# Performance work log

Measured on AMD Instinct MI355X. Metric: run time of the kernel, lower is better.

## Reference

```python
import jax, jax.numpy as jnp
import numpy as np

CROP = 14          # initial_crop_size
POOL_K = 2         # maxpool_kernel_size == maxpool_stride


def setup_inputs() -> dict:
    key = jax.random.key(0)
    k1, k2 = jax.random.split(key)
    features = jax.random.normal(k1, (1, 50, 50, 1024), dtype=jnp.float32)
    raw = jax.random.uniform(k2, (1, 300, 4), dtype=jnp.float32)
    # well-formed normalized boxes: y1<=y2, x1<=x2
    ys = jnp.sort(raw[..., 0::2], axis=-1)
    xs = jnp.sort(raw[..., 1::2], axis=-1)
    boxes = jnp.stack([ys[..., 0], xs[..., 0], ys[..., 1], xs[..., 1]], axis=-1)
    return {"features": features, "boxes": boxes}


def _crop_and_resize(feat, boxes, crop_size):
    # feat: [H, W, C]; boxes: [N, 4] normalized (y1, x1, y2, x2)
    # Matches tf.image.crop_and_resize bilinear semantics for crop_size > 1.
    H, W, _ = feat.shape
    y1, x1, y2, x2 = boxes[:, 0], boxes[:, 1], boxes[:, 2], boxes[:, 3]
    grid = jnp.arange(crop_size, dtype=feat.dtype)  # [S]
    # sample coordinates in source pixel space: [N, S]
    ys = y1[:, None] * (H - 1) + grid[None, :] * ((y2 - y1) * (H - 1) / (crop_size - 1))[:, None]
    xs = x1[:, None] * (W - 1) + grid[None, :] * ((x2 - x1) * (W - 1) / (crop_size - 1))[:, None]
    y0f = jnp.floor(ys)
    x0f = jnp.floor(xs)
    wy = (ys - y0f)[:, :, None, None]  # [N, S, 1, 1]
    wx = (xs - x0f)[:, None, :, None]  # [N, 1, S, 1]
    y0 = jnp.clip(y0f.astype(jnp.int32), 0, H - 1)
    y1i = jnp.clip(y0 + 1, 0, H - 1)
    x0 = jnp.clip(x0f.astype(jnp.int32), 0, W - 1)
    x1i = jnp.clip(x0 + 1, 0, W - 1)
    # four corner gathers -> [N, S, S, C]
    tl = feat[y0[:, :, None], x0[:, None, :]]
    tr = feat[y0[:, :, None], x1i[:, None, :]]
    bl = feat[y1i[:, :, None], x0[:, None, :]]
    br = feat[y1i[:, :, None], x1i[:, None, :]]
    top = tl + (tr - tl) * wx
    bot = bl + (br - bl) * wx
    return top + (bot - top) * wy


def reference(features, boxes):
    # features: [1, H, W, C]; boxes: [1, N, 4]
    crops = _crop_and_resize(features[0], boxes[0], CROP)  # [N, 14, 14, C]
    N, S, _, C = crops.shape
    P = S // POOL_K
    # 2x2 stride-2 max pool (kernel == stride, S even)
    pooled = crops.reshape(N, P, POOL_K, P, POOL_K, C).max(axis=(2, 4))  # [N, 7, 7, C]
    return pooled[None]  # [1, N, 7, 7, C]
```

## Files before the change

kernel.cpp:

```cpp
#include <hip/hip_runtime.h>
#include <math.h>

#define FH 50
#define FW 50
#define FC 1024
#define FC4 256
#define NBOX 300
#define PO 7
#define CHQ 4
#define NPIX (FH * FW * FC)
#define BF16_BYTES (NPIX * 2)

typedef float nat4 __attribute__((ext_vector_type(4)));

__device__ __forceinline__ nat4 lerp4(nat4 a, nat4 b, float w) {
    return a + (b - a) * w;
}
__device__ __forceinline__ nat4 max4(nat4 a, nat4 b) {
    nat4 r;
    r.x = fmaxf(a.x, b.x);
    r.y = fmaxf(a.y, b.y);
    r.z = fmaxf(a.z, b.z);
    r.w = fmaxf(a.w, b.w);
    return r;
}
__device__ __forceinline__ nat4 bf2f(uint2 u) {
    nat4 r;
    r.x = __uint_as_float(u.x << 16);
    r.y = __uint_as_float(u.x & 0xffff0000u);
    r.z = __uint_as_float(u.y << 16);
    r.w = __uint_as_float(u.y & 0xffff0000u);
    return r;
}
__device__ __forceinline__ unsigned bfpack(float a, float b) {
    unsigned ua = __float_as_uint(a);
    unsigned ub = __float_as_uint(b);
    ua += 0x7fffu + ((ua >> 16) & 1u);
    ub += 0x7fffu + ((ub >> 16) & 1u);
    return (ua >> 16) | (ub & 0xffff0000u);
}

__global__ __launch_bounds__(256) void cvt_kernel(
    const float* __restrict__ feat, unsigned* __restrict__ ws)
{
    const int i = blockIdx.x * 256 + threadIdx.x;
    const float4 v = reinterpret_cast<const float4*>(feat)[i];
    uint2 w;
    w.x = bfpack(v.x, v.y);
    w.y = bfpack(v.z, v.w);
    reinterpret_cast<uint2*>(ws)[i] = w;
}

__global__ __launch_bounds__(64) void roi_pool_bf16_kernel(
    const unsigned* __restrict__ ws,
    const float* __restrict__ boxes,
    float* __restrict__ out)
{
    const int j = blockIdx.x & 7;
    const int k = blockIdx.x >> 3;
    const int n = j + 8 * (k / (PO * CHQ));
    if (n >= NBOX) return;
    const int r  = k % (PO * CHQ);
    const int py = r >> 2;
    const int cq = r & 3;
    const int c  = cq * 64 + threadIdx.x;

    const float by1 = boxes[n * 4 + 0];
    const float bx1 = boxes[n * 4 + 1];
    const float by2 = boxes[n * 4 + 2];
    const float bx2 = boxes[n * 4 + 3];

    const float stepy = (by2 - by1) * (49.0f / 13.0f);
    const float stepx = (bx2 - bx1) * (49.0f / 13.0f);
    const float basey = by1 * 49.0f;
    const float basex = bx1 * 49.0f;

    const float ysA = basey + (float)(2 * py) * stepy;
    const float ysB = ysA + stepy;
    const float fA = floorf(ysA); const float wyA = ysA - fA;
    const float fB = floorf(ysB); const float wyB = ysB - fB;
    const int y0A = min(max((int)fA, 0), FH - 1); const int y1A = min(y0A + 1, FH - 1);
    const int y0B = min(max((int)fB, 0), FH - 1); const int y1B = min(y0B + 1, FH - 1);

    const uint2* __restrict__ f2 = reinterpret_cast<const uint2*>(ws);
    const int r0 = y0A * FW, r1 = y1A * FW, r2 = y0B * FW, r3 = y1B * FW;

    uint2 c00, c01, c10, c11, c20, c21, c30, c31;
    uint2 n00, n01, n10, n11, n20, n21, n30, n31;

    int cc;
    {
        const float xf = floorf(basex);
        cc = min(max((int)xf, 0), FW - 1);
        const int x1 = min(cc + 1, FW - 1);
        c00 = f2[(r0 + cc) * FC4 + c];  c01 = f2[(r0 + x1) * FC4 + c];
        c10 = f2[(r1 + cc) * FC4 + c];  c11 = f2[(r1 + x1) * FC4 + c];
        c20 = f2[(r2 + cc) * FC4 + c];  c21 = f2[(r2 + x1) * FC4 + c];
        c30 = f2[(r3 + cc) * FC4 + c];  c31 = f2[(r3 + x1) * FC4 + c];
    }

    nat4 m = (nat4)(-INFINITY);
    nat4* __restrict__ obase =
        reinterpret_cast<nat4*>(out) + (size_t)(n * (PO * PO) + py * PO) * FC4 + c;

    for (int ix = 0; ix < 2 * PO; ++ix) {
        int d = 0;
        if (ix < 2 * PO - 1) {
            const float xsn = basex + (float)(ix + 1) * stepx;
            const int nx0 = min(max((int)floorf(xsn), 0), FW - 1);
            const int nx1 = min(nx0 + 1, FW - 1);
            d = nx0 - cc;
            if (d == 1) {
                n01 = f2[(r0 + nx1) * FC4 + c];
                n11 = f2[(r1 + nx1) * FC4 + c];
                n21 = f2[(r2 + nx1) * FC4 + c];
                n31 = f2[(r3 + nx1) * FC4 + c];
            } else if (d >= 2) {
                n00 = f2[(r0 + nx0) * FC4 + c];  n01 = f2[(r0 + nx1) * FC4 + c];
                n10 = f2[(r1 + nx0) * FC4 + c];  n11 = f2[(r1 + nx1) * FC4 + c];
                n20 = f2[(r2 + nx0) * FC4 + c];  n21 = f2[(r2 + nx1) * FC4 + c];
                n30 = f2[(r3 + nx0) * FC4 + c];  n31 = f2[(r3 + nx1) * FC4 + c];
            }
            cc = nx0;
        }

        {
            const float xs = basex + (float)ix * stepx;
            const float wx = xs - floorf(xs);
            const nat4 vA = lerp4(lerp4(bf2f(c00), bf2f(c01), wx),
                                  lerp4(bf2f(c10), bf2f(c11), wx), wyA);
            const nat4 vB = lerp4(lerp4(bf2f(c20), bf2f(c21), wx),
                                  lerp4(bf2f(c30), bf2f(c31), wx), wyB);
            m = max4(m, max4(vA, vB));
        }

        if (ix & 1) {
            __builtin_nontemporal_store(m, obase + (ix >> 1) * FC4);
            m = (nat4)(-INFINITY);
        }

        if (ix < 2 * PO - 1) {
            if (d == 1) {
                c00 = c01; c10 = c11; c20 = c21; c30 = c31;
                c01 = n01; c11 = n11; c21 = n21; c31 = n31;
            } else if (d >= 2) {
                c00 = n00; c01 = n01; c10 = n10; c11 = n11;
                c20 = n20; c21 = n21; c30 = n30; c31 = n31;
            }
        }
    }
}

__global__ __launch_bounds__(64) void roi_pool_f32_kernel(
    const float* __restrict__ feat,
    const float* __restrict__ boxes,
    float* __restrict__ out)
{
    const int j = blockIdx.x & 7;
    const int k = blockIdx.x >> 3;
    const int n = j + 8 * (k / (PO * CHQ));
    if (n >= NBOX) return;
    const int r  = k % (PO * CHQ);
    const int py = r >> 2;
    const int cq = r & 3;
    const int c4 = cq * 64 + threadIdx.x;

    const float by1 = boxes[n * 4 + 0];
    const float bx1 = boxes[n * 4 + 1];
    const float by2 = boxes[n * 4 + 2];
    const float bx2 = boxes[n * 4 + 3];
    const float stepy = (by2 - by1) * (49.0f / 13.0f);
    const float stepx = (bx2 - bx1) * (49.0f / 13.0f);
    const float basey = by1 * 49.0f;
    const float basex = bx1 * 49.0f;
    const float ysA = basey + (float)(2 * py) * stepy;
    const float ysB = ysA + stepy;
    const float fA = floorf(ysA); const float wyA = ysA - fA;
    const float fB = floorf(ysB); const float wyB = ysB - fB;
    const int y0A = min(max((int)fA, 0), FH - 1); const int y1A = min(y0A + 1, FH - 1);
    const int y0B = min(max((int)fB, 0), FH - 1); const int y1B = min(y0B + 1, FH - 1);

    const nat4* __restrict__ f4 = reinterpret_cast<const nat4*>(feat);
    const int rA0 = y0A * FW, rA1 = y1A * FW, rB0 = y0B * FW, rB1 = y1B * FW;

    int cc = -1000;
    nat4 A00, A01, A10, A11, B00, B01, B10, B11;
    A00 = A01 = A10 = A11 = B00 = B01 = B10 = B11 = (nat4)0.0f;
    nat4 m = (nat4)(-INFINITY);
    nat4* __restrict__ obase =
        reinterpret_cast<nat4*>(out) + (size_t)(n * (PO * PO) + py * PO) * FC4 + c4;

    for (int ix = 0; ix < 2 * PO; ++ix) {
        const float xs = basex + (float)ix * stepx;
        const float xf = floorf(xs);
        const float wx = xs - xf;
        int x0 = min(max((int)xf, 0), FW - 1);
        const int x1 = min(x0 + 1, FW - 1);
        if (x0 != cc) {
            if (x0 == cc + 1) {
                A00 = A01; A10 = A11; B00 = B01; B10 = B11;
                A01 = f4[(rA0 + x1) * FC4 + c4];
                A11 = f4[(rA1 + x1) * FC4 + c4];
                B01 = f4[(rB0 + x1) * FC4 + c4];
                B11 = f4[(rB1 + x1) * FC4 + c4];
            } else {
                A00 = f4[(rA0 + x0) * FC4 + c4];
                A01 = f4[(rA0 + x1) * FC4 + c4];
                A10 = f4[(rA1 + x0) * FC4 + c4];
                A11 = f4[(rA1 + x1) * FC4 + c4];
                B00 = f4[(rB0 + x0) * FC4 + c4];
                B01 = f4[(rB0 + x1) * FC4 + c4];
                B10 = f4[(rB1 + x0) * FC4 + c4];
                B11 = f4[(rB1 + x1) * FC4 + c4];
            }
            cc = x0;
        }
        const nat4 vA = lerp4(lerp4(A00, A01, wx), lerp4(A10, A11, wx), wyA);
        const nat4 vB = lerp4(lerp4(B00, B01, wx), lerp4(B10, B11, wx), wyB);
        m = max4(m, max4(vA, vB));
        if (ix & 1) {
            __builtin_nontemporal_store(m, obase + (ix >> 1) * FC4);
            m = (nat4)(-INFINITY);
        }
    }
}

extern "C" void kernel_launch(void* const* d_in, const int* in_sizes, int n_in,
                              void* d_out, int out_size, void* d_ws, size_t ws_size,
                              hipStream_t stream) {
    const float* feat  = (const float*)d_in[0];
    const float* boxes = (const float*)d_in[1];
    float* out = (float*)d_out;

    dim3 grid(8 * 38 * PO * CHQ);
    dim3 block(64);

    if (ws_size >= (size_t)BF16_BYTES) {
        unsigned* wsb = (unsigned*)d_ws;
        cvt_kernel<<<dim3(NPIX / 4 / 256), dim3(256), 0, stream>>>(feat, wsb);
        roi_pool_bf16_kernel<<<grid, block, 0, stream>>>(wsb, boxes, out);
    } else {
        roi_pool_f32_kernel<<<grid, block, 0, stream>>>(feat, boxes, out);
    }
}
```

Baseline: 98.77 us.

## Split bf16 ROI pool into two channel-half phase launches for cache locality

The bf16 pooling kernel is split into two sequential launches, each covering half of the channel range (512 channels). The block indexing changes from interleaving eight boxes at a time to a simple box-major order with two channel quarters per launch. The intent is to shrink each launch's working set of the bf16 feature map (2.5 MB per half) so gathers hit in L2/MALL more often. It adds an extra kernel launch and drops the box-interleaved scheduling.

```diff
diff --git a/kernel.cpp b/kernel.cpp
--- a/kernel.cpp
+++ b/kernel.cpp
@@ -7,7 +7,6 @@
 #define FC4 256
 #define NBOX 300
 #define PO 7
-#define CHQ 4
 #define NPIX (FH * FW * FC)
 #define BF16_BYTES (NPIX * 2)
 
@@ -51,19 +50,18 @@
     reinterpret_cast<uint2*>(ws)[i] = w;
 }
 
-__global__ __launch_bounds__(64) void roi_pool_bf16_kernel(
+__global__ __launch_bounds__(64) void roi_pool_phase_kernel(
     const unsigned* __restrict__ ws,
     const float* __restrict__ boxes,
-    float* __restrict__ out)
+    float* __restrict__ out,
+    int phase)
 {
-    const int j = blockIdx.x & 7;
-    const int k = blockIdx.x >> 3;
-    const int n = j + 8 * (k / (PO * CHQ));
-    if (n >= NBOX) return;
-    const int r  = k % (PO * CHQ);
-    const int py = r >> 2;
-    const int cq = r & 3;
-    const int c  = cq * 64 + threadIdx.x;
+    const int k   = blockIdx.x;
+    const int cq  = k & 1;
+    const int idx = k >> 1;
+    const int n   = idx / PO;
+    const int py  = idx - n * PO;
+    const int c   = phase * 128 + cq * 64 + threadIdx.x;
 
     const float by1 = boxes[n * 4 + 0];
     const float bx1 = boxes[n * 4 + 1];
@@ -158,9 +156,9 @@
 {
     const int j = blockIdx.x & 7;
     const int k = blockIdx.x >> 3;
-    const int n = j + 8 * (k / (PO * CHQ));
+    const int n = j + 8 * (k / (PO * 4));
     if (n >= NBOX) return;
-    const int r  = k % (PO * CHQ);
+    const int r  = k % (PO * 4);
     const int py = r >> 2;
     const int cq = r & 3;
     const int c4 = cq * 64 + threadIdx.x;
@@ -232,14 +230,16 @@
     const float* boxes = (const float*)d_in[1];
     float* out = (float*)d_out;
 
-    dim3 grid(8 * 38 * PO * CHQ);
-    dim3 block(64);
-
     if (ws_size >= (size_t)BF16_BYTES) {
         unsigned* wsb = (unsigned*)d_ws;
         cvt_kernel<<<dim3(NPIX / 4 / 256), dim3(256), 0, stream>>>(feat, wsb);
-        roi_pool_bf16_kernel<<<grid, block, 0, stream>>>(wsb, boxes, out);
+        dim3 pgrid(NBOX * PO * 2);
+        dim3 pblock(64);
+        roi_pool_phase_kernel<<<pgrid, pblock, 0, stream>>>(wsb, boxes, out, 0);
+        roi_pool_phase_kernel<<<pgrid, pblock, 0, stream>>>(wsb, boxes, out, 1);
     } else {
+        dim3 grid(8 * 38 * PO * 4);
+        dim3 block(64);
         roi_pool_f32_kernel<<<grid, block, 0, stream>>>(feat, boxes, out);
     }
 }
```

Result: slower. 109.6 us (+11.0%).
